# Kernel tuning notes

Hardware: AMD Instinct MI355X
Metric: run time of the kernel (lower is better)

The kernel has to match this reference:

```python
import jax, jax.numpy as jnp
import numpy as np

T, B, D, N = 2048, 16, 1024, 128
EPS = 1e-6


def setup_inputs() -> dict:
    key = jax.random.key(0)
    ks = jax.random.split(key, 6)
    sc = 1.0 / np.sqrt(D)  # ~xavier scale for [N, D] projections
    x = jax.random.normal(ks[0], (T, B, D), jnp.float32)
    S = jnp.zeros((B, N, N), jnp.float32)
    W_k = jax.random.normal(ks[1], (N, D), jnp.float32) * sc
    W_v = jax.random.normal(ks[2], (N, D), jnp.float32) * sc
    W_q = jax.random.normal(ks[3], (N, D), jnp.float32) * sc
    W_beta = jax.random.normal(ks[4], (N, D), jnp.float32) * sc
    d_beta = jnp.full((N,), 0.1, jnp.float32)
    b_beta = jnp.zeros((N,), jnp.float32)
    return {"x": x, "S": S, "W_k": W_k, "W_v": W_v, "W_q": W_q,
            "W_beta": W_beta, "d_beta": d_beta, "b_beta": b_beta}


def reference(x, S, W_k, W_v, W_q, W_beta, d_beta, b_beta):
    # Batched input projections (dense GEMMs over all T*B tokens at once).
    k_all = jnp.einsum('tbd,nd->tbn', x, W_k)
    v_all = jnp.einsum('tbd,nd->tbn', x, W_v)
    q_all = jnp.einsum('tbd,nd->tbn', x, W_q)
    bx_all = jnp.einsum('tbd,nd->tbn', x, W_beta)

    def step(S, inp):
        k, v, q, bx = inp  # each [B, N]
        k_norm = k / (jnp.linalg.norm(k, axis=-1, keepdims=True) + EPS)
        retrieved = jnp.einsum('bij,bj->bi', S, k_norm)
        beta = jax.nn.sigmoid(bx + d_beta * retrieved + b_beta)
        # Delta rule: S += beta * outer(v - retrieved, k_norm)
        S = S + beta[..., None] * ((v - retrieved)[..., None] * k_norm[:, None, :])
        out = jnp.einsum('bij,bj->bi', S, q)
        out = out * jax.nn.silu(out)  # self-gated output
        return S, out

    S_final, outputs = jax.lax.scan(step, S, (k_all, v_all, q_all, bx_all))
    return outputs, S_final
```

## Files before the change

kernel.cpp:

```cpp
#include <hip/hip_runtime.h>
#include <hip/hip_bf16.h>


#define T_STEPS 2048
#define NB 16
#define ND 128
#define KD 1024
#define PSTRIDE 512

typedef __attribute__((ext_vector_type(4))) float f32x4;
typedef __attribute__((ext_vector_type(2))) float f32x2;
typedef __attribute__((ext_vector_type(8))) short short8v;

__device__ __forceinline__ unsigned short f2bf(float f) {
  union { float f; unsigned int u; } c; c.f = f;
  unsigned int u = c.u;
  unsigned int r = u + 0x7fffu + ((u >> 16) & 1u);
  return (unsigned short)(r >> 16);
}

__global__ __launch_bounds__(256) void proj_gemm(
    const float* __restrict__ X,
    const float* __restrict__ Wk, const float* __restrict__ Wv,
    const float* __restrict__ Wq, const float* __restrict__ Wb,
    float* __restrict__ C)
{
  __shared__ unsigned short As[128 * 64];
  __shared__ unsigned short Bs[128 * 64];
  const int tid = threadIdx.x;
  const int bm = blockIdx.x;
  const int bn = blockIdx.y;
  const float* W = (bn == 0) ? Wk : ((bn == 1) ? Wv : ((bn == 2) ? Wq : Wb));
  const int lane = tid & 63;
  const int wave = tid >> 6;
  const int wr = wave >> 1, wc = wave & 1;

  f32x4 acc[4][4];
#pragma unroll
  for (int i = 0; i < 4; i++)
#pragma unroll
    for (int j = 0; j < 4; j++) acc[i][j] = (f32x4){0.f, 0.f, 0.f, 0.f};

  for (int k0 = 0; k0 < KD; k0 += 64) {
    __syncthreads();
#pragma unroll
    for (int c = 0; c < 4; c++) {
      const int g = tid + c * 256;
      const int row = g >> 3;
      const int ch = g & 7;
      const int pos = ((ch ^ (row & 7)) * 8);
      {
        const float* ga = X + (size_t)(bm * 128 + row) * KD + k0 + ch * 8;
        float4 f0 = *(const float4*)(ga);
        float4 f1 = *(const float4*)(ga + 4);
        union { unsigned short u[8]; short8v v; } pk2;
        pk2.u[0] = f2bf(f0.x); pk2.u[1] = f2bf(f0.y);
        pk2.u[2] = f2bf(f0.z); pk2.u[3] = f2bf(f0.w);
        pk2.u[4] = f2bf(f1.x); pk2.u[5] = f2bf(f1.y);
        pk2.u[6] = f2bf(f1.z); pk2.u[7] = f2bf(f1.w);
        *reinterpret_cast<short8v*>(&As[row * 64 + pos]) = pk2.v;
      }
      {
        const float* gb = W + (size_t)row * KD + k0 + ch * 8;
        float4 f0 = *(const float4*)(gb);
        float4 f1 = *(const float4*)(gb + 4);
        union { unsigned short u[8]; short8v v; } pk2;
        pk2.u[0] = f2bf(f0.x); pk2.u[1] = f2bf(f0.y);
        pk2.u[2] = f2bf(f0.z); pk2.u[3] = f2bf(f0.w);
        pk2.u[4] = f2bf(f1.x); pk2.u[5] = f2bf(f1.y);
        pk2.u[6] = f2bf(f1.z); pk2.u[7] = f2bf(f1.w);
        *reinterpret_cast<short8v*>(&Bs[row * 64 + pos]) = pk2.v;
      }
    }
    __syncthreads();
#pragma unroll
    for (int kk = 0; kk < 2; kk++) {
      const int ch = kk * 4 + (lane >> 4);
      short8v a[4], b[4];
#pragma unroll
      for (int i = 0; i < 4; i++) {
        const int ar = wr * 64 + i * 16 + (lane & 15);
        a[i] = *reinterpret_cast<const short8v*>(&As[ar * 64 + ((ch ^ (ar & 7)) * 8)]);
        const int br = wc * 64 + i * 16 + (lane & 15);
        b[i] = *reinterpret_cast<const short8v*>(&Bs[br * 64 + ((ch ^ (br & 7)) * 8)]);
      }
#pragma unroll
      for (int i = 0; i < 4; i++)
#pragma unroll
        for (int j = 0; j < 4; j++)
          acc[i][j] = __builtin_amdgcn_mfma_f32_16x16x32_bf16(a[i], b[j], acc[i][j], 0, 0, 0);
    }
  }
#pragma unroll
  for (int i = 0; i < 4; i++)
#pragma unroll
    for (int j = 0; j < 4; j++)
#pragma unroll
      for (int r = 0; r < 4; r++) {
        const int row = bm * 128 + wr * 64 + i * 16 + (lane >> 4) * 4 + r;
        const int col = bn * 128 + wc * 64 + j * 16 + (lane & 15);
        C[(size_t)row * PSTRIDE + col] = acc[i][j][r];
      }
}

__global__ __launch_bounds__(256) void norm_k(float* __restrict__ proj) {
  const int lane = threadIdx.x & 63;
  const int wid = (blockIdx.x * 256 + threadIdx.x) >> 6;
  float* rowp = proj + (size_t)wid * PSTRIDE;
  float2 kv = *reinterpret_cast<float2*>(rowp + lane * 2);
  float ss = kv.x * kv.x + kv.y * kv.y;
  ss += __shfl_xor(ss, 1);
  ss += __shfl_xor(ss, 2);
  ss += __shfl_xor(ss, 4);
  ss += __shfl_xor(ss, 8);
  ss += __shfl_xor(ss, 16);
  ss += __shfl_xor(ss, 32);
  const float rn = 1.0f / (sqrtf(ss) + 1e-6f);
  kv.x *= rn; kv.y *= rn;
  *reinterpret_cast<float2*>(rowp + lane * 2) = kv;
}

__device__ __forceinline__ float sum16r(float v) {
  v += __int_as_float(__builtin_amdgcn_update_dpp(0, __float_as_int(v), 0x128, 0xF, 0xF, true));
  v += __int_as_float(__builtin_amdgcn_update_dpp(0, __float_as_int(v), 0x124, 0xF, 0xF, true));
  v += __int_as_float(__builtin_amdgcn_update_dpp(0, __float_as_int(v), 0x122, 0xF, 0xF, true));
  v += __int_as_float(__builtin_amdgcn_update_dpp(0, __float_as_int(v), 0x121, 0xF, 0xF, true));
  return v;
}

struct Buf { f32x4 kn0, kn1, q0, q1; float v, bx; };

__device__ __forceinline__ void load_buf_asm(const float* pk, const float* pv, Buf& b) {
  asm volatile("global_load_dwordx4 %0, %1, off"             : "=v"(b.kn0) : "v"(pk));
  asm volatile("global_load_dwordx4 %0, %1, off offset:16"   : "=v"(b.kn1) : "v"(pk));
  asm volatile("global_load_dwordx4 %0, %1, off offset:1024" : "=v"(b.q0)  : "v"(pk));
  asm volatile("global_load_dwordx4 %0, %1, off offset:1040" : "=v"(b.q1)  : "v"(pk));
  asm volatile("global_load_dword %0, %1, off offset:512"    : "=v"(b.v)   : "v"(pv));
  asm volatile("global_load_dword %0, %1, off offset:1536"   : "=v"(b.bx)  : "v"(pv));
}

__device__ __forceinline__ float dot8(const f32x4& a0, const f32x4& a1,
                                      const f32x4& b0, const f32x4& b1) {
  const f32x2 ax = {a0.x, a0.y}, ay = {a0.z, a0.w}, az = {a1.x, a1.y}, aw = {a1.z, a1.w};
  const f32x2 bx = {b0.x, b0.y}, by = {b0.z, b0.w}, bz = {b1.x, b1.y}, bw = {b1.z, b1.w};
  f32x2 p = ax * bx;
  f32x2 q = ay * by;
  p = __builtin_elementwise_fma(az, bz, p);
  q = __builtin_elementwise_fma(aw, bw, q);
  const f32x2 s = p + q;
  return s.x + s.y;
}

__device__ __forceinline__ float dot8S(const f32x2 S2[4], const f32x4& b0, const f32x4& b1) {
  const f32x2 bx = {b0.x, b0.y}, by = {b0.z, b0.w}, bz = {b1.x, b1.y}, bw = {b1.z, b1.w};
  f32x2 p = S2[0] * bx;
  f32x2 q = S2[1] * by;
  p = __builtin_elementwise_fma(S2[2], bz, p);
  q = __builtin_elementwise_fma(S2[3], bw, q);
  const f32x2 s = p + q;
  return s.x + s.y;
}

__device__ __forceinline__ float fin(float od) {
  return od * od * __builtin_amdgcn_rcpf(1.0f + __expf(-od));
}

__global__ __launch_bounds__(64) void scan_kernel(
    const float* __restrict__ proj, const float* __restrict__ S_in,
    const float* __restrict__ d_beta, const float* __restrict__ b_beta,
    float* __restrict__ out, float* __restrict__ S_out)
{
  const int lane = threadIdx.x & 63;
  const int batch = blockIdx.x & 15;
  const int grp = blockIdx.x >> 4;
  const int cc = lane & 15;
  const int rloc = lane >> 4;
  const int row = grp * 4 + rloc;
  const bool w0 = (cc == 0);

  f32x2 S2[4];
  {
    const f32x4* Sp4 = reinterpret_cast<const f32x4*>(
        S_in + ((size_t)batch * ND + row) * ND + cc * 8);
    const f32x4 s0 = Sp4[0], s1 = Sp4[1];
    S2[0] = (f32x2){s0.x, s0.y}; S2[1] = (f32x2){s0.z, s0.w};
    S2[2] = (f32x2){s1.x, s1.y}; S2[3] = (f32x2){s1.z, s1.w};
  }
  const float db = d_beta[row];
  const float bb = b_beta[row];

  const float* pb = proj + (size_t)batch * PSTRIDE;
  const float* pkb = pb + cc * 8;
  const float* pvb = pb + row;
  const size_t sstep = (size_t)NB * PSTRIDE;
  float* outp = out + (size_t)batch * ND + row;
  const size_t ostep = (size_t)NB * ND;

  Buf B0, B1, B2, B3, B4, B5, B6, B7;
  load_buf_asm(pkb + 0 * sstep, pvb + 0 * sstep, B0);
  load_buf_asm(pkb + 1 * sstep, pvb + 1 * sstep, B1);
  load_buf_asm(pkb + 2 * sstep, pvb + 2 * sstep, B2);
  load_buf_asm(pkb + 3 * sstep, pvb + 3 * sstep, B3);
  load_buf_asm(pkb + 4 * sstep, pvb + 4 * sstep, B4);
  load_buf_asm(pkb + 5 * sstep, pvb + 5 * sstep, B5);
  load_buf_asm(pkb + 6 * sstep, pvb + 6 * sstep, B6);
  load_buf_asm(pkb + 7 * sstep, pvb + 7 * sstep, B7);

#define WAIT36 do { asm volatile("s_waitcnt vmcnt(36)" ::: "memory"); \
                    __builtin_amdgcn_sched_barrier(0); } while (0)

  WAIT36;
  float pre0 = sum16r(dot8S(S2, B0.kn0, B0.kn1));
  float kkp = 0.f, crp = 0.f;

#define SLOT(CUR, NXT, tnext)                                             \
  do {                                                                    \
    WAIT36;                                                               \
                       \
    const float d_pre = dot8S(S2, NXT.kn0, NXT.kn1);                      \
    const float d_sq  = dot8S(S2, CUR.q0, CUR.q1);                        \
    const float d_kk  = dot8(CUR.kn0, CUR.kn1, NXT.kn0, NXT.kn1);         \
    const float d_kq  = dot8(CUR.kn0, CUR.kn1, CUR.q0, CUR.q1);           \
    const float pre1 = sum16r(d_pre);                                     \
    const float Sq   = sum16r(d_sq);                                      \
    const float kk   = sum16r(d_kk);                                      \
    const float kq   = sum16r(d_kq);                                      \
                                                        \
    const float r  = fmaf(crp, kkp, pre0);                                \
    const float lg = fmaf(db, r, CUR.bx + bb);                            \
    const float beta = __builtin_amdgcn_rcpf(1.0f + __expf(-lg));         \
    const float cr = beta * (CUR.v - r);                                  \
                                         \
    const float od = fmaf(cr, kq, Sq);                                    \
    if (w0) *outp = fin(od);                                              \
    outp += ostep;                                                        \
                                                            \
    {                                                                     \
      const f32x2 cr2 = {cr, cr};                                         \
      const f32x2 kx = {CUR.kn0.x, CUR.kn0.y}, ky = {CUR.kn0.z, CUR.kn0.w}; \
      const f32x2 kz = {CUR.kn1.x, CUR.kn1.y}, kw = {CUR.kn1.z, CUR.kn1.w}; \
      S2[0] = __builtin_elementwise_fma(cr2, kx, S2[0]);                  \
      S2[1] = __builtin_elementwise_fma(cr2, ky, S2[1]);                  \
      S2[2] = __builtin_elementwise_fma(cr2, kz, S2[2]);                  \
      S2[3] = __builtin_elementwise_fma(cr2, kw, S2[3]);                  \
    }                                                                     \
    pre0 = pre1; kkp = kk; crp = cr;                                      \
    load_buf_asm(pkb + (size_t)(tnext) * sstep,                           \
                 pvb + (size_t)(tnext) * sstep, CUR);                     \
  } while (0)

  for (int t = 0; t < T_STEPS; t += 8) {
    const int t0 = (t +  8 < T_STEPS) ? t +  8 : T_STEPS - 1;
    const int t1 = (t +  9 < T_STEPS) ? t +  9 : T_STEPS - 1;
    const int t2 = (t + 10 < T_STEPS) ? t + 10 : T_STEPS - 1;
    const int t3 = (t + 11 < T_STEPS) ? t + 11 : T_STEPS - 1;
    const int t4 = (t + 12 < T_STEPS) ? t + 12 : T_STEPS - 1;
    const int t5 = (t + 13 < T_STEPS) ? t + 13 : T_STEPS - 1;
    const int t6 = (t + 14 < T_STEPS) ? t + 14 : T_STEPS - 1;
    const int t7 = (t + 15 < T_STEPS) ? t + 15 : T_STEPS - 1;
    SLOT(B0, B1, t0);
    SLOT(B1, B2, t1);
    SLOT(B2, B3, t2);
    SLOT(B3, B4, t3);
    SLOT(B4, B5, t4);
    SLOT(B5, B6, t5);
    SLOT(B6, B7, t6);
    SLOT(B7, B0, t7);
  }
#undef SLOT
#undef WAIT36

  asm volatile("s_waitcnt vmcnt(0)" ::: "memory");
  {
    f32x4* So4 = reinterpret_cast<f32x4*>(
        S_out + ((size_t)batch * ND + row) * ND + cc * 8);
    f32x4 s0, s1;
    s0.x = S2[0].x; s0.y = S2[0].y; s0.z = S2[1].x; s0.w = S2[1].y;
    s1.x = S2[2].x; s1.y = S2[2].y; s1.z = S2[3].x; s1.w = S2[3].y;
    So4[0] = s0; So4[1] = s1;
  }
}

extern "C" void kernel_launch(void* const* d_in, const int* in_sizes, int n_in,
                              void* d_out, int out_size, void* d_ws, size_t ws_size,
                              hipStream_t stream) {
  const float* x  = (const float*)d_in[0];
  const float* S0 = (const float*)d_in[1];
  const float* Wk = (const float*)d_in[2];
  const float* Wv = (const float*)d_in[3];
  const float* Wq = (const float*)d_in[4];
  const float* Wb = (const float*)d_in[5];
  const float* db = (const float*)d_in[6];
  const float* bb = (const float*)d_in[7];
  float* out  = (float*)d_out;
  float* Sout = out + (size_t)T_STEPS * NB * ND;
  float* proj = (float*)d_ws;

  dim3 ggrid(256, 4);
  proj_gemm<<<ggrid, 256, 0, stream>>>(x, Wk, Wv, Wq, Wb, proj);
  norm_k<<<8192, 256, 0, stream>>>(proj);
  scan_kernel<<<512, 64, 0, stream>>>(proj, S0, db, bb, out, Sout);
}
```

Before: 426.0 us.

## Map one S row per wavefront with full 64-lane reductions in scan

Restructures the recurrent scan so each 64-lane wavefront owns a single row of S (two columns per lane) instead of four rows with sixteen lanes each. The launch grows from 512 to 2048 blocks, and each lane's per-step loads and register state shrink. The output dot product is now computed directly after the S update instead of through the precomputed kq/Sq algebraic shortcut. Each step now runs three full-wave reductions that need cross-row shuffles on the serial dependency chain, and the four-fold larger grid issues more redundant loads of k and q.

```diff
diff --git a/kernel.cpp b/kernel.cpp
--- a/kernel.cpp
+++ b/kernel.cpp
@@ -120,45 +120,23 @@
   *reinterpret_cast<float2*>(rowp + lane * 2) = kv;
 }
 
-__device__ __forceinline__ float sum16r(float v) {
+__device__ __forceinline__ float sum64(float v) {
+  v += __int_as_float(__builtin_amdgcn_update_dpp(0, __float_as_int(v), 0x121, 0xF, 0xF, true));
+  v += __int_as_float(__builtin_amdgcn_update_dpp(0, __float_as_int(v), 0x122, 0xF, 0xF, true));
+  v += __int_as_float(__builtin_amdgcn_update_dpp(0, __float_as_int(v), 0x124, 0xF, 0xF, true));
   v += __int_as_float(__builtin_amdgcn_update_dpp(0, __float_as_int(v), 0x128, 0xF, 0xF, true));
-  v += __int_as_float(__builtin_amdgcn_update_dpp(0, __float_as_int(v), 0x124, 0xF, 0xF, true));
-  v += __int_as_float(__builtin_amdgcn_update_dpp(0, __float_as_int(v), 0x122, 0xF, 0xF, true));
-  v += __int_as_float(__builtin_amdgcn_update_dpp(0, __float_as_int(v), 0x121, 0xF, 0xF, true));
+  v += __shfl_xor(v, 16);
+  v += __shfl_xor(v, 32);
   return v;
 }
 
-struct Buf { f32x4 kn0, kn1, q0, q1; float v, bx; };
+struct Buf { f32x2 kn, q; float v, bx; };
 
 __device__ __forceinline__ void load_buf_asm(const float* pk, const float* pv, Buf& b) {
-  asm volatile("global_load_dwordx4 %0, %1, off"             : "=v"(b.kn0) : "v"(pk));
-  asm volatile("global_load_dwordx4 %0, %1, off offset:16"   : "=v"(b.kn1) : "v"(pk));
-  asm volatile("global_load_dwordx4 %0, %1, off offset:1024" : "=v"(b.q0)  : "v"(pk));
-  asm volatile("global_load_dwordx4 %0, %1, off offset:1040" : "=v"(b.q1)  : "v"(pk));
-  asm volatile("global_load_dword %0, %1, off offset:512"    : "=v"(b.v)   : "v"(pv));
-  asm volatile("global_load_dword %0, %1, off offset:1536"   : "=v"(b.bx)  : "v"(pv));
-}
-
-__device__ __forceinline__ float dot8(const f32x4& a0, const f32x4& a1,
-                                      const f32x4& b0, const f32x4& b1) {
-  const f32x2 ax = {a0.x, a0.y}, ay = {a0.z, a0.w}, az = {a1.x, a1.y}, aw = {a1.z, a1.w};
-  const f32x2 bx = {b0.x, b0.y}, by = {b0.z, b0.w}, bz = {b1.x, b1.y}, bw = {b1.z, b1.w};
-  f32x2 p = ax * bx;
-  f32x2 q = ay * by;
-  p = __builtin_elementwise_fma(az, bz, p);
-  q = __builtin_elementwise_fma(aw, bw, q);
-  const f32x2 s = p + q;
-  return s.x + s.y;
-}
-
-__device__ __forceinline__ float dot8S(const f32x2 S2[4], const f32x4& b0, const f32x4& b1) {
-  const f32x2 bx = {b0.x, b0.y}, by = {b0.z, b0.w}, bz = {b1.x, b1.y}, bw = {b1.z, b1.w};
-  f32x2 p = S2[0] * bx;
-  f32x2 q = S2[1] * by;
-  p = __builtin_elementwise_fma(S2[2], bz, p);
-  q = __builtin_elementwise_fma(S2[3], bw, q);
-  const f32x2 s = p + q;
-  return s.x + s.y;
+  asm volatile("global_load_dwordx2 %0, %1, off"             : "=v"(b.kn) : "v"(pk));
+  asm volatile("global_load_dwordx2 %0, %1, off offset:1024" : "=v"(b.q)  : "v"(pk));
+  asm volatile("global_load_dword %0, %1, off"               : "=v"(b.v)  : "v"(pv));
+  asm volatile("global_load_dword %0, %1, off offset:1024"   : "=v"(b.bx) : "v"(pv));
 }
 
 __device__ __forceinline__ float fin(float od) {
@@ -172,26 +150,17 @@
 {
   const int lane = threadIdx.x & 63;
   const int batch = blockIdx.x & 15;
-  const int grp = blockIdx.x >> 4;
-  const int cc = lane & 15;
-  const int rloc = lane >> 4;
-  const int row = grp * 4 + rloc;
-  const bool w0 = (cc == 0);
-
-  f32x2 S2[4];
-  {
-    const f32x4* Sp4 = reinterpret_cast<const f32x4*>(
-        S_in + ((size_t)batch * ND + row) * ND + cc * 8);
-    const f32x4 s0 = Sp4[0], s1 = Sp4[1];
-    S2[0] = (f32x2){s0.x, s0.y}; S2[1] = (f32x2){s0.z, s0.w};
-    S2[2] = (f32x2){s1.x, s1.y}; S2[3] = (f32x2){s1.z, s1.w};
-  }
+  const int row = blockIdx.x >> 4;
+  const bool w0 = (lane == 0);
+
+  f32x2 S2 = *reinterpret_cast<const f32x2*>(
+      S_in + ((size_t)batch * ND + row) * ND + lane * 2);
   const float db = d_beta[row];
   const float bb = b_beta[row];
 
   const float* pb = proj + (size_t)batch * PSTRIDE;
-  const float* pkb = pb + cc * 8;
-  const float* pvb = pb + row;
+  const float* pkb = pb + lane * 2;
+  const float* pvb = pb + 128 + row;
   const size_t sstep = (size_t)NB * PSTRIDE;
   float* outp = out + (size_t)batch * ND + row;
   const size_t ostep = (size_t)NB * ND;
@@ -206,45 +175,38 @@
   load_buf_asm(pkb + 6 * sstep, pvb + 6 * sstep, B6);
   load_buf_asm(pkb + 7 * sstep, pvb + 7 * sstep, B7);
 
-#define WAIT36 do { asm volatile("s_waitcnt vmcnt(36)" ::: "memory"); \
+#define WAIT24 do { asm volatile("s_waitcnt vmcnt(24)" ::: "memory"); \
                     __builtin_amdgcn_sched_barrier(0); } while (0)
 
-  WAIT36;
-  float pre0 = sum16r(dot8S(S2, B0.kn0, B0.kn1));
+  WAIT24;
+  float pre0;
+  {
+    const f32x2 p = S2 * B0.kn;
+    pre0 = sum64(p.x + p.y);
+  }
   float kkp = 0.f, crp = 0.f;
 
 #define SLOT(CUR, NXT, tnext)                                             \
   do {                                                                    \
-    WAIT36;                                                               \
-                       \
-    const float d_pre = dot8S(S2, NXT.kn0, NXT.kn1);                      \
-    const float d_sq  = dot8S(S2, CUR.q0, CUR.q1);                        \
-    const float d_kk  = dot8(CUR.kn0, CUR.kn1, NXT.kn0, NXT.kn1);         \
-    const float d_kq  = dot8(CUR.kn0, CUR.kn1, CUR.q0, CUR.q1);           \
-    const float pre1 = sum16r(d_pre);                                     \
-    const float Sq   = sum16r(d_sq);                                      \
-    const float kk   = sum16r(d_kk);                                      \
-    const float kq   = sum16r(d_kq);                                      \
+    WAIT24;                                                               \
+                          \
+    const f32x2 dp = S2 * NXT.kn;                                         \
+    const f32x2 dk = CUR.kn * NXT.kn;                                     \
+    const float pre1 = sum64(dp.x + dp.y);                                \
+    const float kk1  = sum64(dk.x + dk.y);                                \
                                                         \
     const float r  = fmaf(crp, kkp, pre0);                                \
     const float lg = fmaf(db, r, CUR.bx + bb);                            \
     const float beta = __builtin_amdgcn_rcpf(1.0f + __expf(-lg));         \
     const float cr = beta * (CUR.v - r);                                  \
-                                         \
-    const float od = fmaf(cr, kq, Sq);                                    \
+                                          \
+    const f32x2 cr2 = {cr, cr};                                           \
+    S2 = __builtin_elementwise_fma(cr2, CUR.kn, S2);                      \
+    const f32x2 ov = S2 * CUR.q;                                          \
+    const float od = sum64(ov.x + ov.y);                                  \
     if (w0) *outp = fin(od);                                              \
     outp += ostep;                                                        \
-                                                            \
-    {                                                                     \
-      const f32x2 cr2 = {cr, cr};                                         \
-      const f32x2 kx = {CUR.kn0.x, CUR.kn0.y}, ky = {CUR.kn0.z, CUR.kn0.w}; \
-      const f32x2 kz = {CUR.kn1.x, CUR.kn1.y}, kw = {CUR.kn1.z, CUR.kn1.w}; \
-      S2[0] = __builtin_elementwise_fma(cr2, kx, S2[0]);                  \
-      S2[1] = __builtin_elementwise_fma(cr2, ky, S2[1]);                  \
-      S2[2] = __builtin_elementwise_fma(cr2, kz, S2[2]);                  \
-      S2[3] = __builtin_elementwise_fma(cr2, kw, S2[3]);                  \
-    }                                                                     \
-    pre0 = pre1; kkp = kk; crp = cr;                                      \
+    pre0 = pre1; kkp = kk1; crp = cr;                                     \
     load_buf_asm(pkb + (size_t)(tnext) * sstep,                           \
                  pvb + (size_t)(tnext) * sstep, CUR);                     \
   } while (0)
@@ -268,17 +230,11 @@
     SLOT(B7, B0, t7);
   }
 #undef SLOT
-#undef WAIT36
+#undef WAIT24
 
   asm volatile("s_waitcnt vmcnt(0)" ::: "memory");
-  {
-    f32x4* So4 = reinterpret_cast<f32x4*>(
-        S_out + ((size_t)batch * ND + row) * ND + cc * 8);
-    f32x4 s0, s1;
-    s0.x = S2[0].x; s0.y = S2[0].y; s0.z = S2[1].x; s0.w = S2[1].y;
-    s1.x = S2[2].x; s1.y = S2[2].y; s1.z = S2[3].x; s1.w = S2[3].y;
-    So4[0] = s0; So4[1] = s1;
-  }
+  *reinterpret_cast<f32x2*>(
+      S_out + ((size_t)batch * ND + row) * ND + lane * 2) = S2;
 }
 
 extern "C" void kernel_launch(void* const* d_in, const int* in_sizes, int n_in,
@@ -299,5 +255,5 @@
   dim3 ggrid(256, 4);
   proj_gemm<<<ggrid, 256, 0, stream>>>(x, Wk, Wv, Wq, Wb, proj);
   norm_k<<<8192, 256, 0, stream>>>(proj);
-  scan_kernel<<<512, 64, 0, stream>>>(proj, S0, db, bb, out, Sout);
-}
+  scan_kernel<<<2048, 64, 0, stream>>>(proj, S0, db, bb, out, Sout);
+}
```

Result: slower. 691.8 us (+62.4%).
